# Kernel optimization log

Hardware: AMD Instinct MI355X
Metric: run time of the kernel (lower is better)

Reference implementation:

```python
import jax, jax.numpy as jnp
import numpy as np

WIDTH = 4096
NUM_HEADS = 8
BLOCK_W = WIDTH // NUM_HEADS


def _block_diag_linear(x, w, b):
    # x: [n, width] -> [n, h, bw]; w: [h, bw, bw]; b: [h, bw]
    n = x.shape[0]
    xh = x.reshape(n, NUM_HEADS, BLOCK_W)
    y = jnp.einsum('nhi,hij->nhj', xh, w) + b
    return y.reshape(n, WIDTH)


def setup_inputs() -> dict:
    key = jax.random.key(0)
    ks = jax.random.split(key, 7)
    n = 8192
    x = jax.random.normal(ks[0], (n, WIDTH), dtype=jnp.float32)
    s = jnp.sort(jax.random.randint(ks[1], (n,), 0, 8, dtype=jnp.int32))
    # a_param init: uniform on ring radii [0.9, 0.999], softplus-inverse transform
    eps = 1e-8
    u = jax.random.uniform(ks[2], (WIDTH,), minval=0.9**2 + eps, maxval=0.999**2 + eps)
    t = 0.5 * jnp.log(u)
    a_param = jnp.log(jnp.exp(-t) - 1.0).astype(jnp.float32)
    std = 1.0 / np.sqrt(BLOCK_W)
    ig_w = std * jax.random.normal(ks[3], (NUM_HEADS, BLOCK_W, BLOCK_W), dtype=jnp.float32)
    ig_b = jnp.zeros((NUM_HEADS, BLOCK_W), dtype=jnp.float32)
    ag_w = std * jax.random.normal(ks[4], (NUM_HEADS, BLOCK_W, BLOCK_W), dtype=jnp.float32)
    ag_b = jnp.zeros((NUM_HEADS, BLOCK_W), dtype=jnp.float32)
    return {'x': x, 's': s, 'a_param': a_param, 'ig_w': ig_w, 'ig_b': ig_b,
            'ag_w': ag_w, 'ag_b': ag_b}


def reference(x, s, a_param, ig_w, ig_b, ag_w, ag_b):
    n, k = x.shape
    # reset mask: True at position 0 and wherever segment id changes
    reset = jnp.concatenate([jnp.ones((1,), dtype=bool), s[1:] != s[:-1]])
    gate_x = jax.nn.sigmoid(_block_diag_linear(x, ig_w, ig_b))
    gate_a = jax.nn.sigmoid(_block_diag_linear(x, ag_w, ag_b))
    log_a = -8.0 * gate_a * jax.nn.softplus(a_param)  # [n, k]
    a = jnp.exp(log_a)
    a_square = jnp.exp(2.0 * log_a)
    multiplier = jnp.sqrt(1.0 - a_square)
    multiplier = jnp.where(reset[:, None], 1.0, multiplier)
    normalized_x = x * gate_x * multiplier
    # linear recurrence h[t] = a[t] * h[t-1] + normalized_x[t] via parallel scan
    def combine(e1, e2):
        a1, b1 = e1
        a2, b2 = e2
        return (a1 * a2, a2 * b1 + b2)
    _, out = jax.lax.associative_scan(combine, (a, normalized_x), axis=0)
    return out
```

## Files before the change

kernel.cpp:

```cpp
#include <hip/hip_runtime.h>
#include <hip/hip_bf16.h>
#include <stdint.h>

#define WIDTH 4096
#define NROWS 8192
#define NHEADS 8
#define BW 512
#define CS 128
#define NCHUNK (NROWS/CS)

typedef short bf16x8 __attribute__((ext_vector_type(8)));
typedef float f32x4 __attribute__((ext_vector_type(4)));

__device__ __forceinline__ uint32_t rne_bf16(float f) {
  uint32_t u = __float_as_uint(f);
  return (u + 0x7fffu + ((u >> 16) & 1u)) >> 16;
}
__device__ __forceinline__ uint32_t pack2(float lo, float hi) {
  return rne_bf16(lo) | (rne_bf16(hi) << 16);
}
__device__ __forceinline__ float bf16_to_f32(uint32_t bits) {
  return __uint_as_float(bits << 16);
}

__device__ __forceinline__ void gload_lds16(const void* g, void* l) {
  __builtin_amdgcn_global_load_lds(
      (const __attribute__((address_space(1))) void*)g,
      (__attribute__((address_space(3))) void*)l, 16, 0, 0);
}

__global__ void prep_xbf16(const float* __restrict__ x, uint16_t* __restrict__ xb) {
  size_t i = ((size_t)blockIdx.x * 256 + threadIdx.x) * 8;
  float4 f0 = *reinterpret_cast<const float4*>(x + i);
  float4 f1 = *reinterpret_cast<const float4*>(x + i + 4);
  uint4 v;
  v.x = pack2(f0.x, f0.y); v.y = pack2(f0.z, f0.w);
  v.z = pack2(f1.x, f1.y); v.w = pack2(f1.z, f1.w);
  *reinterpret_cast<uint4*>(xb + i) = v;
}

__global__ void prep_weights(const float* __restrict__ ig_w,
                             const float* __restrict__ ag_w,
                             uint16_t* __restrict__ wt) {
  __shared__ float tile[32][33];
  int j0 = blockIdx.x * 32;
  int i0 = blockIdx.y * 32;
  int m  = blockIdx.z;
  const float* src = ((m >> 3) ? ag_w : ig_w) + (size_t)(m & 7) * BW * BW;
  int tx = threadIdx.x & 31, ty = threadIdx.x >> 5;
  #pragma unroll
  for (int k = 0; k < 4; k++) {
    int i = i0 + ty + 8 * k;
    tile[ty + 8 * k][tx] = src[(size_t)i * BW + (j0 + tx)];
  }
  __syncthreads();
  #pragma unroll
  for (int k = 0; k < 4; k++) {
    int j = j0 + ty + 8 * k;
    wt[((size_t)m * BW + j) * BW + (i0 + tx)] = (uint16_t)rne_bf16(tile[tx][ty + 8 * k]);
  }
}

__global__ void prep_misc(const float* __restrict__ a_param, float* __restrict__ cvec) {
  int i = blockIdx.x * 256 + threadIdx.x;
  if (i < WIDTH) {
    float x = a_param[i];
    float sp = (x > 15.f) ? x : log1pf(expf(x));
    cvec[i] = 8.f * sp;
  }
}

#define BM 256
#define BN 128
#define BK 64

__global__ __launch_bounds__(512, 2)
void gates_gemm(const uint16_t* __restrict__ xb,
                const int* __restrict__ s,
                const uint16_t* __restrict__ wt,
                const float* __restrict__ ig_b,
                const float* __restrict__ ag_b,
                const float* __restrict__ cvec,
                uint32_t* __restrict__ lanx,
                float* __restrict__ cA,
                float* __restrict__ cB) {
  extern __shared__ __align__(16) unsigned char dsm[];
  __shared__ unsigned char resetm[BM];

  const int b = blockIdx.x;
  const int orig = (b & 7) * 128 + (b >> 3);
  const int h  = orig >> 7;
  const int rem = orig & 127;
  const int mt = rem >> 2;
  const int nt = rem & 3;
  const int m0 = mt * BM;
  const int j0 = nt * BN;

  const int tid = threadIdx.x;
  const int lane = tid & 63;
  const int w = tid >> 6;
  const int wr = w >> 1;
  const int wc = w & 1;
  const int lrow = lane & 15;
  const int lkg  = lane >> 4;

  if (tid < BM) {
    int n = m0 + tid;
    resetm[tid] = (n == 0) || (s[n] != s[n - 1]);
  }

  const char* xb_src[4];
  #pragma unroll
  for (int i = 0; i < 4; i++) {
    int o = (4 * w + i) * 1024 + (lane << 4);
    int row = o >> 7;
    int c = (o & 127) ^ ((row & 7) << 4);
    xb_src[i] = (const char*)xb + (size_t)(m0 + row) * (WIDTH * 2) + h * (BW * 2) + c;
  }
  const char* w_src[4];
  #pragma unroll
  for (int i = 0; i < 4; i++) {
    int o = (4 * w + i) * 1024 + (lane << 4);
    int g = o >> 14;
    int jl = (o >> 7) & 127;
    int c = (o & 127) ^ ((jl & 7) << 4);
    w_src[i] = (const char*)wt + ((size_t)((g * 8 + h) * BW + (j0 + jl))) * (BW * 2) + c;
  }

  f32x4 acc[2][4][4];
  #pragma unroll
  for (int g = 0; g < 2; g++)
    #pragma unroll
    for (int mf = 0; mf < 4; mf++)
      #pragma unroll
      for (int nf = 0; nf < 4; nf++)
        acc[g][mf][nf] = (f32x4){0.f, 0.f, 0.f, 0.f};

  #pragma unroll
  for (int i = 0; i < 4; i++)
    gload_lds16(xb_src[i], dsm + (4 * w + i) * 1024);
  #pragma unroll
  for (int i = 0; i < 4; i++)
    gload_lds16(w_src[i], dsm + 32768 + (4 * w + i) * 1024);
  __syncthreads();

  for (int kt = 0; kt < 8; kt++) {
    const uint32_t cbase = (uint32_t)(kt & 1) << 16;
    if (kt < 7) {
      const uint32_t nbase = cbase ^ 65536u;
      #pragma unroll
      for (int i = 0; i < 4; i++)
        gload_lds16(xb_src[i] + (kt + 1) * 128, dsm + nbase + (4 * w + i) * 1024);
      #pragma unroll
      for (int i = 0; i < 4; i++)
        gload_lds16(w_src[i] + (kt + 1) * 128, dsm + nbase + 32768 + (4 * w + i) * 1024);
    }
    #pragma unroll
    for (int ks = 0; ks < 2; ks++) {
      bf16x8 af[4];
      #pragma unroll
      for (int mf = 0; mf < 4; mf++) {
        int row = wr * 64 + 16 * mf + lrow;
        uint32_t addr = cbase + (uint32_t)((row << 7) + ks * 64 + lkg * 16);
        addr ^= (uint32_t)((row & 7) << 4);
        af[mf] = *reinterpret_cast<const bf16x8*>(dsm + addr);
      }
      #pragma unroll
      for (int g = 0; g < 2; g++) {
        #pragma unroll
        for (int nf = 0; nf < 4; nf++) {
          int j = wc * 64 + 16 * nf + lrow;
          uint32_t addr = cbase + (uint32_t)(32768 + (g << 14) + (j << 7) + ks * 64 + lkg * 16);
          addr ^= (uint32_t)((j & 7) << 4);
          bf16x8 bfr = *reinterpret_cast<const bf16x8*>(dsm + addr);
          #pragma unroll
          for (int mf = 0; mf < 4; mf++) {
            acc[g][mf][nf] = __builtin_amdgcn_mfma_f32_16x16x32_bf16(
                af[mf], bfr, acc[g][mf][nf], 0, 0, 0);
          }
        }
      }
    }
    __syncthreads();
  }

  float* smf = (float*)dsm;

  #pragma unroll
  for (int nf = 0; nf < 4; nf++) {
    int j = j0 + wc * 64 + 16 * nf + lrow;
    int jj = h * BW + j;
    float igb = ig_b[jj], agb = ag_b[jj], cv = cvec[jj];
    float segA[4], segB[4];
    #pragma unroll
    for (int mf = 0; mf < 4; mf++) {
      float A = 1.f, B = 0.f;
      int nbase = m0 + wr * 64 + 16 * mf + 4 * lkg;
      #pragma unroll
      for (int r = 0; r < 4; r++) {
        int n = nbase + r;
        size_t o = (size_t)n * WIDTH + jj;
        float yig = acc[0][mf][nf][r] + igb;
        float yag = acc[1][mf][nf][r] + agb;
        float gx = __builtin_amdgcn_rcpf(1.f + __expf(-yig));
        float ga = __builtin_amdgcn_rcpf(1.f + __expf(-yag));
        float la = -ga * cv;
        uint32_t la_bits = rne_bf16(la);
        float la_r = bf16_to_f32(la_bits);
        float a = __expf(la_r);
        float mult = resetm[n - m0] ? 1.f
                     : __builtin_amdgcn_sqrtf(fmaxf(1.f - a * a, 0.f));
        float xv = bf16_to_f32((uint32_t)xb[o]);
        float nx = xv * gx * mult;
        uint32_t nx_bits = rne_bf16(nx);
        float nx_r = bf16_to_f32(nx_bits);
        lanx[o] = la_bits | (nx_bits << 16);
        A *= a;
        B = fmaf(a, B, nx_r);
      }
      segA[mf] = A; segB[mf] = B;
    }
    #pragma unroll
    for (int mf = 0; mf < 4; mf++) {
      float A = segA[mf], B = segB[mf];
      #pragma unroll
      for (int d = 16; d <= 32; d <<= 1) {
        float pA = __shfl_xor(A, d, 64);
        float pB = __shfl_xor(B, d, 64);
        bool up = (lane & d) != 0;
        B = up ? fmaf(A, pB, B) : fmaf(pA, B, pB);
        A *= pA;
      }
      segA[mf] = A; segB[mf] = B;
    }
    float colA = segA[0], colB = segB[0];
    #pragma unroll
    for (int mf = 1; mf < 4; mf++) {
      colB = fmaf(segA[mf], colB, segB[mf]);
      colA *= segA[mf];
    }
    if (lkg == 0) {
      int clocal = wc * 64 + 16 * nf + lrow;
      smf[wr * 128 + clocal] = colA;
      smf[512 + wr * 128 + clocal] = colB;
    }
  }
  __syncthreads();
  if (tid < 256) {
    int half = tid >> 7;
    int cl = tid & 127;
    int base = half * 2;
    float A0 = smf[base * 128 + cl],       B0 = smf[512 + base * 128 + cl];
    float A1 = smf[(base + 1) * 128 + cl], B1 = smf[512 + (base + 1) * 128 + cl];
    float Af = A0 * A1;
    float Bf = fmaf(A1, B0, B1);
    int ct = mt * 2 + half;
    int jj = h * BW + j0 + cl;
    cA[ct * WIDTH + jj] = Af;
    cB[ct * WIDTH + jj] = Bf;
  }
}

__global__ void scan_prefix(const float* __restrict__ cA, const float* __restrict__ cB,
                            float* __restrict__ prefix) {
  int c = blockIdx.x * 256 + threadIdx.x;
  float hcur = 0.f;
  for (int i0 = 0; i0 < NCHUNK; i0 += 8) {
    float av[8], bv[8];
    #pragma unroll
    for (int e = 0; e < 8; e++) { av[e] = cA[(i0 + e) * WIDTH + c]; bv[e] = cB[(i0 + e) * WIDTH + c]; }
    #pragma unroll
    for (int e = 0; e < 8; e++) { prefix[(i0 + e) * WIDTH + c] = hcur; hcur = av[e] * hcur + bv[e]; }
  }
}

__global__ void scan_apply(const uint32_t* __restrict__ lanx,
                           const float* __restrict__ prefix,
                           float* __restrict__ out) {
  int chunk = blockIdx.x;
  int c0 = (blockIdx.y * 256 + threadIdx.x) * 4;
  size_t base = (size_t)chunk * CS * WIDTH + c0;
  float h[4];
  #pragma unroll
  for (int q = 0; q < 4; q++) h[q] = prefix[chunk * WIDTH + c0 + q];
  for (int rb = 0; rb < CS; rb += 4) {
    uint4 v[4];
    #pragma unroll
    for (int e = 0; e < 4; e++)
      v[e] = *reinterpret_cast<const uint4*>(lanx + base + (size_t)(rb + e) * WIDTH);
    #pragma unroll
    for (int e = 0; e < 4; e++) {
      float4 ov;
      h[0] = fmaf(__expf(bf16_to_f32(v[e].x & 0xffffu)), h[0], bf16_to_f32(v[e].x >> 16)); ov.x = h[0];
      h[1] = fmaf(__expf(bf16_to_f32(v[e].y & 0xffffu)), h[1], bf16_to_f32(v[e].y >> 16)); ov.y = h[1];
      h[2] = fmaf(__expf(bf16_to_f32(v[e].z & 0xffffu)), h[2], bf16_to_f32(v[e].z >> 16)); ov.z = h[2];
      h[3] = fmaf(__expf(bf16_to_f32(v[e].w & 0xffffu)), h[3], bf16_to_f32(v[e].w >> 16)); ov.w = h[3];
      *reinterpret_cast<float4*>(out + base + (size_t)(rb + e) * WIDTH) = ov;
    }
  }
}

extern "C" void kernel_launch(void* const* d_in, const int* in_sizes, int n_in,
                              void* d_out, int out_size, void* d_ws, size_t ws_size,
                              hipStream_t stream) {
  const float* x       = (const float*)d_in[0];
  const int*   s       = (const int*)d_in[1];
  const float* a_param = (const float*)d_in[2];
  const float* ig_w    = (const float*)d_in[3];
  const float* ig_b    = (const float*)d_in[4];
  const float* ag_w    = (const float*)d_in[5];
  const float* ag_b    = (const float*)d_in[6];
  float* out = (float*)d_out;
  char* ws = (char*)d_ws;

  uint32_t* lanx   = (uint32_t*)ws;
  uint16_t* wt     = (uint16_t*)(ws + 134217728);
  uint16_t* xb     = (uint16_t*)(ws + 142606336);
  float*    cvec   = (float*)(ws + 209715200);
  float*    cA     = (float*)(ws + 209731584);
  float*    cB     = (float*)(ws + 210780160);
  float*    prefix = (float*)(ws + 211828736);

  prep_xbf16<<<dim3(16384), 256, 0, stream>>>(x, xb);
  prep_weights<<<dim3(16, 16, 16), 256, 0, stream>>>(ig_w, ag_w, wt);
  prep_misc<<<dim3(16), 256, 0, stream>>>(a_param, cvec);
  gates_gemm<<<dim3(1024), dim3(512), 131072, stream>>>(xb, s, wt, ig_b, ag_b, cvec,
                                                        lanx, cA, cB);
  scan_prefix<<<dim3(16), 256, 0, stream>>>(cA, cB, prefix);
  scan_apply<<<dim3(NCHUNK, 4), 256, 0, stream>>>(lanx, prefix, out);
}
```

Before: 219.5 us.

## Fuse fp32-to-bf16 conversion of x into the gates GEMM loader

Drops the separate prep_xbf16 pass and its bf16 copy of x. The GEMM now loads fp32 x through registers, converts it to bf16 and writes it into swizzled LDS, which removes a full read and write of x plus a launch. The K-loop starts at a rotated offset per N-tile to spread reads, and the epilogue reads x from the LDS tile it already holds instead of global memory. In exchange, the x path loses the async global-to-LDS copy and raises register use, and each of the four N-tile blocks per row range now reads twice as many fp32 bytes of x.

```diff
diff --git a/kernel.cpp b/kernel.cpp
--- a/kernel.cpp
+++ b/kernel.cpp
@@ -27,16 +27,6 @@
   __builtin_amdgcn_global_load_lds(
       (const __attribute__((address_space(1))) void*)g,
       (__attribute__((address_space(3))) void*)l, 16, 0, 0);
-}
-
-__global__ void prep_xbf16(const float* __restrict__ x, uint16_t* __restrict__ xb) {
-  size_t i = ((size_t)blockIdx.x * 256 + threadIdx.x) * 8;
-  float4 f0 = *reinterpret_cast<const float4*>(x + i);
-  float4 f1 = *reinterpret_cast<const float4*>(x + i + 4);
-  uint4 v;
-  v.x = pack2(f0.x, f0.y); v.y = pack2(f0.z, f0.w);
-  v.z = pack2(f1.x, f1.y); v.w = pack2(f1.z, f1.w);
-  *reinterpret_cast<uint4*>(xb + i) = v;
 }
 
 __global__ void prep_weights(const float* __restrict__ ig_w,
@@ -75,7 +65,7 @@
 #define BK 64
 
 __global__ __launch_bounds__(512, 2)
-void gates_gemm(const uint16_t* __restrict__ xb,
+void gates_gemm(const float* __restrict__ x,
                 const int* __restrict__ s,
                 const uint16_t* __restrict__ wt,
                 const float* __restrict__ ig_b,
@@ -109,14 +99,16 @@
     resetm[tid] = (n == 0) || (s[n] != s[n - 1]);
   }
 
-  const char* xb_src[4];
-  #pragma unroll
-  for (int i = 0; i < 4; i++) {
-    int o = (4 * w + i) * 1024 + (lane << 4);
-    int row = o >> 7;
-    int c = (o & 127) ^ ((row & 7) << 4);
-    xb_src[i] = (const char*)xb + (size_t)(m0 + row) * (WIDTH * 2) + h * (BW * 2) + c;
-  }
+  const int xrow = tid >> 1;
+  const int xhalf = tid & 1;
+  const float* xrow_ptr = x + (size_t)(m0 + xrow) * WIDTH + h * BW + xhalf * 32;
+  uint32_t xw_addr[4];
+  #pragma unroll
+  for (int q = 0; q < 4; q++) {
+    uint32_t o = (uint32_t)(tid * 64 + q * 16);
+    xw_addr[q] = o ^ (uint32_t)((xrow & 7) << 4);
+  }
+
   const char* w_src[4];
   #pragma unroll
   for (int i = 0; i < 4; i++) {
@@ -136,24 +128,45 @@
       for (int nf = 0; nf < 4; nf++)
         acc[g][mf][nf] = (f32x4){0.f, 0.f, 0.f, 0.f};
 
-  #pragma unroll
-  for (int i = 0; i < 4; i++)
-    gload_lds16(xb_src[i], dsm + (4 * w + i) * 1024);
-  #pragma unroll
-  for (int i = 0; i < 4; i++)
-    gload_lds16(w_src[i], dsm + 32768 + (4 * w + i) * 1024);
+  {
+    const int p0 = (2 * nt + 2) & 7;
+    const float* xp = xrow_ptr + p0 * 64;
+    float4 xf[8];
+    #pragma unroll
+    for (int q = 0; q < 4; q++) {
+      xf[2 * q]     = *reinterpret_cast<const float4*>(xp + q * 8);
+      xf[2 * q + 1] = *reinterpret_cast<const float4*>(xp + q * 8 + 4);
+    }
+    #pragma unroll
+    for (int i = 0; i < 4; i++)
+      gload_lds16(w_src[i] + p0 * 128, dsm + 32768 + (4 * w + i) * 1024);
+    #pragma unroll
+    for (int q = 0; q < 4; q++) {
+      uint4 v;
+      v.x = pack2(xf[2 * q].x,     xf[2 * q].y);
+      v.y = pack2(xf[2 * q].z,     xf[2 * q].w);
+      v.z = pack2(xf[2 * q + 1].x, xf[2 * q + 1].y);
+      v.w = pack2(xf[2 * q + 1].z, xf[2 * q + 1].w);
+      *reinterpret_cast<uint4*>(dsm + xw_addr[q]) = v;
+    }
+  }
   __syncthreads();
 
-  for (int kt = 0; kt < 8; kt++) {
-    const uint32_t cbase = (uint32_t)(kt & 1) << 16;
-    if (kt < 7) {
-      const uint32_t nbase = cbase ^ 65536u;
-      #pragma unroll
-      for (int i = 0; i < 4; i++)
-        gload_lds16(xb_src[i] + (kt + 1) * 128, dsm + nbase + (4 * w + i) * 1024);
-      #pragma unroll
-      for (int i = 0; i < 4; i++)
-        gload_lds16(w_src[i] + (kt + 1) * 128, dsm + nbase + 32768 + (4 * w + i) * 1024);
+  for (int i = 0; i < 8; i++) {
+    const uint32_t cbase = (uint32_t)(i & 1) << 16;
+    const uint32_t nbase = cbase ^ 65536u;
+    float4 xf[8];
+    if (i < 7) {
+      const int p = (2 * nt + 3 + i) & 7;
+      const float* xp = xrow_ptr + p * 64;
+      #pragma unroll
+      for (int q = 0; q < 4; q++) {
+        xf[2 * q]     = *reinterpret_cast<const float4*>(xp + q * 8);
+        xf[2 * q + 1] = *reinterpret_cast<const float4*>(xp + q * 8 + 4);
+      }
+      #pragma unroll
+      for (int q = 0; q < 4; q++)
+        gload_lds16(w_src[q] + p * 128, dsm + nbase + 32768 + (4 * w + q) * 1024);
     }
     #pragma unroll
     for (int ks = 0; ks < 2; ks++) {
@@ -181,24 +194,38 @@
         }
       }
     }
+    if (i < 7) {
+      #pragma unroll
+      for (int q = 0; q < 4; q++) {
+        uint4 v;
+        v.x = pack2(xf[2 * q].x,     xf[2 * q].y);
+        v.y = pack2(xf[2 * q].z,     xf[2 * q].w);
+        v.z = pack2(xf[2 * q + 1].x, xf[2 * q + 1].y);
+        v.w = pack2(xf[2 * q + 1].z, xf[2 * q + 1].w);
+        *reinterpret_cast<uint4*>(dsm + nbase + xw_addr[q]) = v;
+      }
+    }
     __syncthreads();
   }
 
-  float* smf = (float*)dsm;
+  float* smf = (float*)(dsm + 98304);
 
   #pragma unroll
   for (int nf = 0; nf < 4; nf++) {
-    int j = j0 + wc * 64 + 16 * nf + lrow;
-    int jj = h * BW + j;
+    int jl = wc * 64 + 16 * nf + lrow;
+    int jj = h * BW + j0 + jl;
+    const uint32_t xsl = (uint32_t)(jl >> 6) << 16;
+    const int cc2 = (jl & 63) * 2;
     float igb = ig_b[jj], agb = ag_b[jj], cv = cvec[jj];
     float segA[4], segB[4];
     #pragma unroll
     for (int mf = 0; mf < 4; mf++) {
       float A = 1.f, B = 0.f;
-      int nbase = m0 + wr * 64 + 16 * mf + 4 * lkg;
+      int rbase = wr * 64 + 16 * mf + 4 * lkg;
       #pragma unroll
       for (int r = 0; r < 4; r++) {
-        int n = nbase + r;
+        int row = rbase + r;
+        int n = m0 + row;
         size_t o = (size_t)n * WIDTH + jj;
         float yig = acc[0][mf][nf][r] + igb;
         float yag = acc[1][mf][nf][r] + agb;
@@ -208,9 +235,10 @@
         uint32_t la_bits = rne_bf16(la);
         float la_r = bf16_to_f32(la_bits);
         float a = __expf(la_r);
-        float mult = resetm[n - m0] ? 1.f
+        float mult = resetm[row] ? 1.f
                      : __builtin_amdgcn_sqrtf(fmaxf(1.f - a * a, 0.f));
-        float xv = bf16_to_f32((uint32_t)xb[o]);
+        uint32_t xaddr = xsl + ((uint32_t)((row << 7) + cc2) ^ (uint32_t)((row & 7) << 4));
+        float xv = bf16_to_f32(*reinterpret_cast<const uint16_t*>(dsm + xaddr));
         float nx = xv * gx * mult;
         uint32_t nx_bits = rne_bf16(nx);
         float nx_r = bf16_to_f32(nx_bits);
@@ -315,16 +343,14 @@
 
   uint32_t* lanx   = (uint32_t*)ws;
   uint16_t* wt     = (uint16_t*)(ws + 134217728);
-  uint16_t* xb     = (uint16_t*)(ws + 142606336);
-  float*    cvec   = (float*)(ws + 209715200);
-  float*    cA     = (float*)(ws + 209731584);
-  float*    cB     = (float*)(ws + 210780160);
-  float*    prefix = (float*)(ws + 211828736);
-
-  prep_xbf16<<<dim3(16384), 256, 0, stream>>>(x, xb);
+  float*    cvec   = (float*)(ws + 142606336);
+  float*    cA     = (float*)(ws + 142622720);
+  float*    cB     = (float*)(ws + 143671296);
+  float*    prefix = (float*)(ws + 144719872);
+
   prep_weights<<<dim3(16, 16, 16), 256, 0, stream>>>(ig_w, ag_w, wt);
   prep_misc<<<dim3(16), 256, 0, stream>>>(a_param, cvec);
-  gates_gemm<<<dim3(1024), dim3(512), 131072, stream>>>(xb, s, wt, ig_b, ag_b, cvec,
+  gates_gemm<<<dim3(1024), dim3(512), 131072, stream>>>(x, s, wt, ig_b, ag_b, cvec,
                                                         lanx, cA, cB);
   scan_prefix<<<dim3(16), 256, 0, stream>>>(cA, cB, prefix);
   scan_apply<<<dim3(NCHUNK, 4), 256, 0, stream>>>(lanx, prefix, out);
```

Measured after the change: 239.8 us. 9.3% more time.

## Rotate K-tile order so the epilogue reads x from the resident LDS tile

Applied to the files above, without the earlier changes.

The K-loop now starts at a tile offset derived from the column tile index nt, so the last tile loaded into LDS covers the same x columns this block writes in its epilogue. The epilogue then reads x values from that swizzled LDS buffer instead of doing a second scattered global load of xb, and the float scratch area moves to a separate LDS offset so it does not overwrite that data. This saves global traffic in the epilogue. The rotated start also staggers K-tile access across blocks, at the cost of extra address arithmetic and a dependence on the exact buffer and swizzle mapping.

```diff
diff --git a/kernel.cpp b/kernel.cpp
--- a/kernel.cpp
+++ b/kernel.cpp
@@ -136,24 +136,28 @@
       for (int nf = 0; nf < 4; nf++)
         acc[g][mf][nf] = (f32x4){0.f, 0.f, 0.f, 0.f};
 
-  #pragma unroll
-  for (int i = 0; i < 4; i++)
-    gload_lds16(xb_src[i], dsm + (4 * w + i) * 1024);
-  #pragma unroll
-  for (int i = 0; i < 4; i++)
-    gload_lds16(w_src[i], dsm + 32768 + (4 * w + i) * 1024);
+  {
+    const int p0 = (2 * nt + 2) & 7;
+    #pragma unroll
+    for (int i = 0; i < 4; i++)
+      gload_lds16(xb_src[i] + p0 * 128, dsm + (4 * w + i) * 1024);
+    #pragma unroll
+    for (int i = 0; i < 4; i++)
+      gload_lds16(w_src[i] + p0 * 128, dsm + 32768 + (4 * w + i) * 1024);
+  }
   __syncthreads();
 
   for (int kt = 0; kt < 8; kt++) {
     const uint32_t cbase = (uint32_t)(kt & 1) << 16;
     if (kt < 7) {
       const uint32_t nbase = cbase ^ 65536u;
+      const int p = (2 * nt + 3 + kt) & 7;
       #pragma unroll
       for (int i = 0; i < 4; i++)
-        gload_lds16(xb_src[i] + (kt + 1) * 128, dsm + nbase + (4 * w + i) * 1024);
+        gload_lds16(xb_src[i] + p * 128, dsm + nbase + (4 * w + i) * 1024);
       #pragma unroll
       for (int i = 0; i < 4; i++)
-        gload_lds16(w_src[i] + (kt + 1) * 128, dsm + nbase + 32768 + (4 * w + i) * 1024);
+        gload_lds16(w_src[i] + p * 128, dsm + nbase + 32768 + (4 * w + i) * 1024);
     }
     #pragma unroll
     for (int ks = 0; ks < 2; ks++) {
@@ -184,21 +188,24 @@
     __syncthreads();
   }
 
-  float* smf = (float*)dsm;
+  float* smf = (float*)(dsm + 98304);
 
   #pragma unroll
   for (int nf = 0; nf < 4; nf++) {
-    int j = j0 + wc * 64 + 16 * nf + lrow;
-    int jj = h * BW + j;
+    int jl = wc * 64 + 16 * nf + lrow;
+    int jj = h * BW + j0 + jl;
+    const uint32_t xsl = (uint32_t)(jl >> 6) << 16;
+    const int cc2 = (jl & 63) * 2;
     float igb = ig_b[jj], agb = ag_b[jj], cv = cvec[jj];
     float segA[4], segB[4];
     #pragma unroll
     for (int mf = 0; mf < 4; mf++) {
       float A = 1.f, B = 0.f;
-      int nbase = m0 + wr * 64 + 16 * mf + 4 * lkg;
+      int rbase = wr * 64 + 16 * mf + 4 * lkg;
       #pragma unroll
       for (int r = 0; r < 4; r++) {
-        int n = nbase + r;
+        int row = rbase + r;
+        int n = m0 + row;
         size_t o = (size_t)n * WIDTH + jj;
         float yig = acc[0][mf][nf][r] + igb;
         float yag = acc[1][mf][nf][r] + agb;
@@ -208,9 +215,10 @@
         uint32_t la_bits = rne_bf16(la);
         float la_r = bf16_to_f32(la_bits);
         float a = __expf(la_r);
-        float mult = resetm[n - m0] ? 1.f
+        float mult = resetm[row] ? 1.f
                      : __builtin_amdgcn_sqrtf(fmaxf(1.f - a * a, 0.f));
-        float xv = bf16_to_f32((uint32_t)xb[o]);
+        uint32_t xaddr = xsl + ((uint32_t)((row << 7) + cc2) ^ (uint32_t)((row & 7) << 4));
+        float xv = bf16_to_f32(*reinterpret_cast<const uint16_t*>(dsm + xaddr));
         float nx = xv * gx * mult;
         uint32_t nx_bits = rne_bf16(nx);
         float nx_r = bf16_to_f32(nx_bits);
```

New measurement: 236.1 us. 7.6% more time.
